# Kernel tuning notes

Measured on AMD Instinct MI355X. Metric: run time of the kernel, lower is better.

The kernel has to match this reference:

```python
import jax, jax.numpy as jnp
import numpy as np

N, IN_DIM, OUT_DIM, NUM_HOPS, SD = 8192, 256, 256, 4, 64
ETA, LAM_LAP, LAM_SP, EPS = 0.5, 0.3, 0.05, 0.5
LN_EPS = 1e-5


def setup_inputs() -> dict:
    key = jax.random.key(0)
    ks = jax.random.split(key, 6)
    K = NUM_HOPS + 1
    return {
        "H": jax.random.normal(ks[0], (N, IN_DIM), jnp.float32),
        "hops": jax.random.normal(ks[1], (K, N, IN_DIM), jnp.float32),
        "L": jax.random.normal(ks[2], (N, N), jnp.float32),
        "U": jax.random.normal(ks[3], (K, IN_DIM, SD), jnp.float32) * 0.1,
        "W_in": jax.random.normal(ks[4], (OUT_DIM, IN_DIM), jnp.float32) * 0.05,
        "ln_gamma": jnp.ones((OUT_DIM,), jnp.float32),
        "ln_beta": jnp.zeros((OUT_DIM,), jnp.float32),
        "log_tau": jnp.zeros((), jnp.float32),
    }


def _per_hop(U_k, H_k):
    n = H_k.shape[0]
    Q, _ = jnp.linalg.qr(U_k)                 # [in_dim, sd]
    Z = Q.T @ H_k.T                           # [sd, n]
    G = Z @ Z.T                               # [sd, sd] Gram, reused
    Sigma = G / (n + 1e-8)
    tr_S = jnp.trace(Sigma)
    tr_S2 = jnp.sum(Sigma * Sigma)            # trace(Sigma @ Sigma), Sigma symmetric
    rank_eff = tr_S ** 2 / (tr_S2 + 1e-8)
    coeff = SD / (n * EPS ** 2 + 1e-8)
    M = jnp.eye(SD, dtype=Z.dtype) + coeff * G
    Lc = jnp.linalg.cholesky(M)
    MiZ = jax.scipy.linalg.cho_solve((Lc, True), Z)  # [sd, n]
    grad_R = (Q @ MiZ).T                      # [n, in_dim]
    return rank_eff, grad_R


def reference(H, hops, L, U, W_in, ln_gamma, ln_beta, log_tau):
    tau = jnp.clip(jnp.exp(log_tau), 0.1, 10.0)
    rank_effs, grads_R = jax.vmap(_per_hop)(U, hops)      # [K], [K,n,in_dim]
    lap_terms = jnp.einsum('nm,kmd->knd', L, hops)        # [K,n,in_dim]
    w = jax.nn.softmax(rank_effs / tau)                   # [K]
    grad_sum = jnp.einsum('k,knd->nd', w, grads_R)
    lap_sum = jnp.einsum('k,knd->nd', w, lap_terms)
    H_half = H + ETA * grad_sum - ETA * LAM_LAP * lap_sum
    H_prox = jnp.sign(H_half) * jax.nn.relu(jnp.abs(H_half) - LAM_SP * ETA)
    H_out = H_prox @ W_in.T
    mu = jnp.mean(H_out, axis=-1, keepdims=True)
    var = jnp.var(H_out, axis=-1, keepdims=True)
    H_out = (H_out - mu) * jax.lax.rsqrt(var + LN_EPS) * ln_gamma + ln_beta
    return H_out, rank_effs, w
```

## Files before the change

kernel.cpp:

```cpp
#include <hip/hip_runtime.h>
#include <stdint.h>


typedef __attribute__((ext_vector_type(8))) short  s16x8;
typedef __attribute__((ext_vector_type(4))) float  f32x4;

#define NNODE 8192
#define DIN   256
#define KHOP  5
#define SDM   64

static const size_t OFF_Q    = 0;
static const size_t OFF_QT   = OFF_Q   + (size_t)5*256*64*4;
static const size_t OFF_ZT   = OFF_QT  + (size_t)5*64*256*2;
static const size_t OFF_GP   = OFF_ZT  + (size_t)5*8192*64*2;
static const size_t OFF_LM   = OFF_GP  + (size_t)5*16*4096*4;
static const size_t OFF_RD   = OFF_LM  + (size_t)5*4096*4;
static const size_t OFF_LU   = OFF_RD  + (size_t)5*64*4;
static const size_t OFF_RDU  = OFF_LU  + (size_t)5*4096*4;
static const size_t OFF_RE   = OFF_RDU + (size_t)5*64*4;
static const size_t OFF_W    = OFF_RE  + 64;
static const size_t OFF_T2   = OFF_W   + 64;
static const size_t OFF_HWT  = OFF_T2  + (size_t)5*256*64*2;
static const size_t OFF_WBF  = OFF_HWT + (size_t)256*8192*2;
static const size_t OFF_HP   = OFF_WBF + (size_t)256*256*2;
static const size_t OFF_PART = OFF_HP  + (size_t)8192*256*2;

__device__ __forceinline__ unsigned short f2bf(float f){
  unsigned u = __builtin_bit_cast(unsigned, f);
  u += 0x7FFFu + ((u >> 16) & 1u);
  return (unsigned short)(u >> 16);
}
__device__ __forceinline__ float bf2f(unsigned h){
  return __builtin_bit_cast(float, h << 16);
}
__device__ __forceinline__ void gl_lds16(const void* g, void* l){
  __builtin_amdgcn_global_load_lds(
      (const __attribute__((address_space(1))) void*)g,
      (__attribute__((address_space(3))) void*)l, 16, 0, 0);
}
__device__ __forceinline__ f32x4 mfma16(s16x8 a, s16x8 b, f32x4 c){
  return __builtin_amdgcn_mfma_f32_16x16x32_bf16(a, b, c, 0, 0, 0);
}
__device__ __forceinline__ int swz(int row7, int colbyte){
  return row7*128 + (colbyte ^ (row7 << 4));
}

__device__ __forceinline__ void wave_chol64(float* a, float& rdk, int lane){
  rdk = 0.0f;
  #pragma unroll
  for (int j = 0; j < 64; ++j){
    float dj  = __shfl(a[j], j);
    float d   = sqrtf(fmaxf(dj, 1e-20f));
    float rdj = 1.0f / d;
    float cj  = a[j] * rdj;
    a[j] = cj;
    if (lane == j) rdk = rdj;
    #pragma unroll
    for (int l = j+1; l < 64; ++l)
      a[l] -= cj * __shfl(cj, l);
  }
}

__global__ __launch_bounds__(256) void k_pre(const float* __restrict__ U,
                                             float* __restrict__ Lu,
                                             float* __restrict__ rdu){
  __shared__ float A[64*65];
  int tid = threadIdx.x;
  int k = blockIdx.x;
  const float* Uk = U + (size_t)k*16384;
  int ti = tid >> 4, tj = tid & 15;
  float s[16];
  #pragma unroll
  for (int i = 0; i < 16; ++i) s[i] = 0.0f;
  for (int n = 0; n < 256; ++n){
    f32x4 xa = *(const f32x4*)(Uk + n*64 + ti*4);
    f32x4 xb = *(const f32x4*)(Uk + n*64 + tj*4);
    #pragma unroll
    for (int p = 0; p < 4; ++p)
      #pragma unroll
      for (int q = 0; q < 4; ++q) s[p*4+q] += xa[p]*xb[q];
  }
  #pragma unroll
  for (int p = 0; p < 4; ++p)
    #pragma unroll
    for (int q = 0; q < 4; ++q) A[(ti*4+p)*65 + tj*4+q] = s[p*4+q];
  __syncthreads();
  if (tid < 64){
    int lane = tid;
    float a[64];
    #pragma unroll
    for (int l = 0; l < 64; ++l) a[l] = A[lane*65 + l];
    float rdk;
    wave_chol64(a, rdk, lane);
    #pragma unroll
    for (int l = 0; l < 64; ++l) Lu[(size_t)k*4096 + lane*64 + l] = a[l];
    rdu[k*64 + lane] = rdk;
  }
}

__global__ __launch_bounds__(256) void k_qsolve(const float* __restrict__ U,
                                                const float* __restrict__ Lu,
                                                const float* __restrict__ rdu,
                                                float* __restrict__ Qf,
                                                unsigned short* __restrict__ Qt){
  int k = blockIdx.y, tid = threadIdx.x, wave = tid >> 6, lane = tid & 63;
  __shared__ float Al[64*65];
  __shared__ float rds[64];
  for (int e = tid; e < 4096; e += 256) Al[(e>>6)*65 + (e&63)] = Lu[(size_t)k*4096 + e];
  if (tid < 64) rds[tid] = rdu[k*64 + tid];
  __syncthreads();
  int n = blockIdx.x*4 + wave;
  float x = U[((size_t)k*256 + n)*64 + lane];
  #pragma unroll
  for (int j = 0; j < 64; ++j){
    float zj = __shfl(x, j) * rds[j];
    x = (lane == j) ? zj : (lane > j ? x - Al[lane*65+j]*zj : x);
  }
  Qf[((size_t)k*256 + n)*64 + lane] = x;
  Qt[(size_t)k*16384 + lane*256 + n] = f2bf(x);
}

__global__ __launch_bounds__(256,2) void k_zgemm(const float* __restrict__ hops,
                                                 const unsigned short* __restrict__ Qt,
                                                 unsigned short* __restrict__ Zt){
  __shared__ __align__(16) unsigned short Al[128][72];
  __shared__ __align__(16) unsigned short Bl[64][64];
  int tid = threadIdx.x, lane = tid & 63, wave = tid >> 6;
  int q = lane >> 4, r = lane & 15;
  int k = blockIdx.y, m0 = blockIdx.x * 128;
  f32x4 acc[2][4];
  #pragma unroll
  for (int a = 0; a < 2; ++a)
    #pragma unroll
    for (int b = 0; b < 4; ++b) acc[a][b] = (f32x4){0,0,0,0};
  int rr = tid >> 1, half = tid & 1;
  for (int it = 0; it < 4; ++it){
    __syncthreads();
    #pragma unroll
    for (int i = 0; i < 2; ++i){
      int o = i*4096 + wave*1024 + lane*16;
      int srow = o >> 7, kc = (o & 127) >> 1;
      gl_lds16(Qt + (size_t)k*16384 + srow*256 + it*64 + kc,
               (char*)&Bl[0][0] + i*4096 + wave*1024);
    }
    const float* ga = hops + ((size_t)k*NNODE + m0 + rr)*256 + it*64 + half*32;
    f32x4 v[8];
    #pragma unroll
    for (int i = 0; i < 8; ++i) v[i] = *(const f32x4*)(ga + i*4);
    #pragma unroll
    for (int i = 0; i < 4; ++i){
      s16x8 t;
      #pragma unroll
      for (int j = 0; j < 8; ++j){ int e = i*8+j; t[j] = (short)f2bf(v[e>>2][e&3]); }
      *(s16x8*)&Al[rr][half*32 + i*8] = t;
    }
    __syncthreads();
    #pragma unroll
    for (int h = 0; h < 2; ++h){
      int ko = h*32 + q*8;
      s16x8 b[4];
      #pragma unroll
      for (int ni = 0; ni < 4; ++ni) b[ni] = *(const s16x8*)&Bl[ni*16 + r][ko];
      #pragma unroll
      for (int mi = 0; mi < 2; ++mi){
        s16x8 a = *(const s16x8*)&Al[wave*32 + mi*16 + r][ko];
        #pragma unroll
        for (int ni = 0; ni < 4; ++ni) acc[mi][ni] = mfma16(a, b[ni], acc[mi][ni]);
      }
    }
  }
  #pragma unroll
  for (int mi = 0; mi < 2; ++mi)
    #pragma unroll
    for (int ni = 0; ni < 4; ++ni)
      #pragma unroll
      for (int ii = 0; ii < 4; ++ii){
        int m = m0 + wave*32 + mi*16 + q*4 + ii;
        int sc = ni*16 + r;
        Zt[((size_t)k*NNODE + m)*64 + sc] = f2bf(acc[mi][ni][ii]);
      }
}

__global__ __launch_bounds__(256) void k_gpart(const unsigned short* __restrict__ Zt,
                                               float* __restrict__ Gp){
  int k = blockIdx.x, c = blockIdx.y, tid = threadIdx.x;
  __shared__ __align__(16) unsigned short Zl[128][64];
  int ti = tid >> 4, tj = tid & 15;
  float acc[16];
  #pragma unroll
  for (int i = 0; i < 16; ++i) acc[i] = 0.0f;
  for (int sub = 0; sub < 4; ++sub){
    const char* gb = (const char*)Zt + ((size_t)k*NNODE + c*512 + sub*128)*128;
    __syncthreads();
    #pragma unroll
    for (int i = 0; i < 4; ++i){
      int o = i*4096 + tid*16;
      *(uint4*)((char*)&Zl[0][0] + o) = *(const uint4*)(gb + o);
    }
    __syncthreads();
    for (int n = 0; n < 128; ++n){
      const unsigned short* row = &Zl[n][0];
      uint2 ua = *(const uint2*)(row + ti*4);
      uint2 ub = *(const uint2*)(row + tj*4);
      float xa[4] = { bf2f(ua.x & 0xffff), bf2f(ua.x >> 16), bf2f(ua.y & 0xffff), bf2f(ua.y >> 16) };
      float xb[4] = { bf2f(ub.x & 0xffff), bf2f(ub.x >> 16), bf2f(ub.y & 0xffff), bf2f(ub.y >> 16) };
      #pragma unroll
      for (int p = 0; p < 4; ++p)
        #pragma unroll
        for (int qn = 0; qn < 4; ++qn) acc[p*4+qn] += xa[p]*xb[qn];
    }
  }
  float* o = Gp + ((size_t)k*16 + c)*4096;
  #pragma unroll
  for (int p = 0; p < 4; ++p)
    #pragma unroll
    for (int qn = 0; qn < 4; ++qn) o[(ti*4+p)*64 + tj*4+qn] = acc[p*4+qn];
}

__global__ __launch_bounds__(256) void k_gred(const float* __restrict__ Gp,
                                              float* __restrict__ LmO,
                                              float* __restrict__ rdO,
                                              float* __restrict__ reO){
  int k = blockIdx.x, tid = threadIdx.x;
  __shared__ float A[64*65];
  __shared__ float red[256];
  int ti = tid >> 4, tj = tid & 15;
  float s[16];
  #pragma unroll
  for (int i = 0; i < 16; ++i) s[i] = 0.0f;
  for (int c = 0; c < 16; ++c){
    const float* g = Gp + ((size_t)k*16 + c)*4096 + (ti*4)*64 + tj*4;
    #pragma unroll
    for (int p = 0; p < 4; ++p)
      #pragma unroll
      for (int qn = 0; qn < 4; ++qn) s[p*4+qn] += g[p*64+qn];
  }
  const float sc    = 1.0f / (8192.0f + 1e-8f);
  const float coeff = 64.0f / (8192.0f*0.25f + 1e-8f);
  float trp = 0.0f, tr2p = 0.0f;
  #pragma unroll
  for (int p = 0; p < 4; ++p)
    #pragma unroll
    for (int qn = 0; qn < 4; ++qn){
      float gg = s[p*4+qn];
      float sg = gg * sc;
      tr2p += sg*sg;
      int row = ti*4+p, col = tj*4+qn;
      if (row == col) trp += sg;
      A[row*65 + col] = (row == col ? 1.0f : 0.0f) + coeff*gg;
    }
  red[tid] = trp; __syncthreads();
  for (int o = 128; o > 0; o >>= 1){ if (tid < o) red[tid] += red[tid+o]; __syncthreads(); }
  float tr = red[0]; __syncthreads();
  red[tid] = tr2p; __syncthreads();
  for (int o = 128; o > 0; o >>= 1){ if (tid < o) red[tid] += red[tid+o]; __syncthreads(); }
  float tr2 = red[0];
  if (tid == 0) reO[k] = tr*tr / (tr2 + 1e-8f);
  __syncthreads();
  if (tid < 64){
    int lane = tid;
    float a[64];
    #pragma unroll
    for (int l = 0; l < 64; ++l) a[l] = A[lane*65 + l];
    float rdk;
    wave_chol64(a, rdk, lane);
    #pragma unroll
    for (int l = 0; l < 64; ++l) LmO[(size_t)k*4096 + lane*64 + l] = a[l];
    rdO[k*64 + lane] = rdk;
  }
}

__global__ void k_soft(const float* __restrict__ re, const float* __restrict__ ltau,
                       float* __restrict__ wv, float* __restrict__ dtail){
  if (threadIdx.x == 0){
    float tau = expf(ltau[0]);
    tau = fminf(fmaxf(tau, 0.1f), 10.0f);
    float r[5], m = -1e30f;
    for (int i = 0; i < 5; ++i){ r[i] = re[i]; m = fmaxf(m, r[i]); }
    float e[5], sum = 0.0f;
    for (int i = 0; i < 5; ++i){ e[i] = expf((r[i]-m)/tau); sum += e[i]; }
    for (int i = 0; i < 5; ++i){
      float w = e[i]/sum;
      wv[i] = w; dtail[i] = r[i]; dtail[5+i] = w;
    }
  }
}

__global__ __launch_bounds__(256) void k_post(const float* __restrict__ hops,
                                              const float* __restrict__ wv,
                                              unsigned short* __restrict__ hwT,
                                              const float* __restrict__ Qf,
                                              const float* __restrict__ LmI,
                                              const float* __restrict__ rdI,
                                              unsigned short* __restrict__ T2w,
                                              const float* __restrict__ Win,
                                              unsigned short* __restrict__ Wbf){
  __shared__ float T[64*65];
  __shared__ float rds[64];
  int bid = blockIdx.x, tid = threadIdx.x;
  if (bid < 512){
    int n0 = (bid & 127)*64, d0 = (bid >> 7)*64;
    float wl[5];
    #pragma unroll
    for (int k = 0; k < 5; ++k) wl[k] = -0.15f * wv[k];
    for (int e = tid; e < 1024; e += 256){
      int row = e >> 4, c4 = (e & 15)*4;
      f32x4 acc = (f32x4){0,0,0,0};
      #pragma unroll
      for (int k = 0; k < 5; ++k){
        f32x4 v = *(const f32x4*)(hops + ((size_t)k*NNODE + n0 + row)*256 + d0 + c4);
        acc += v * wl[k];
      }
      T[row*65 + c4+0] = acc[0]; T[row*65 + c4+1] = acc[1];
      T[row*65 + c4+2] = acc[2]; T[row*65 + c4+3] = acc[3];
    }
    __syncthreads();
    for (int e = tid; e < 1024; e += 256){
      int dr = e >> 4, c4 = (e & 15)*4;
      unsigned short h0 = f2bf(T[(c4+0)*65 + dr]);
      unsigned short h1 = f2bf(T[(c4+1)*65 + dr]);
      unsigned short h2 = f2bf(T[(c4+2)*65 + dr]);
      unsigned short h3 = f2bf(T[(c4+3)*65 + dr]);
      uint2 u; u.x = (unsigned)h0 | ((unsigned)h1 << 16); u.y = (unsigned)h2 | ((unsigned)h3 << 16);
      *(uint2*)(hwT + (size_t)(d0+dr)*NNODE + n0 + c4) = u;
    }
  } else if (bid < 832){
    int i = bid - 512;
    int k = i >> 6, xb = i & 63;
    int wave = tid >> 6, lane = tid & 63;
    for (int e = tid; e < 4096; e += 256) T[(e>>6)*65 + (e&63)] = LmI[(size_t)k*4096 + e];
    if (tid < 64) rds[tid] = rdI[k*64 + tid];
    __syncthreads();
    int n = xb*4 + wave;
    float x = Qf[((size_t)k*256 + n)*64 + lane];
    #pragma unroll
    for (int j = 0; j < 64; ++j){
      float zj = __shfl(x, j) * rds[j];
      x = (lane == j) ? zj : (lane > j ? x - T[lane*65+j]*zj : x);
    }
    #pragma unroll
    for (int j = 63; j >= 0; --j){
      float yj = __shfl(x, j) * rds[j];
      x = (lane == j) ? yj : (lane < j ? x - T[j*65+lane]*yj : x);
    }
    float scale = 0.5f * wv[k];
    T2w[((size_t)k*256 + n)*64 + lane] = f2bf(scale * x);
  } else {
    int i = bid - 832;
    int e = (i*256 + tid)*4;
    f32x4 v = *(const f32x4*)(Win + e);
    uint2 u;
    u.x = (unsigned)f2bf(v[0]) | ((unsigned)f2bf(v[1]) << 16);
    u.y = (unsigned)f2bf(v[2]) | ((unsigned)f2bf(v[3]) << 16);
    *(uint2*)(Wbf + e) = u;
  }
}

__global__ __launch_bounds__(256,2) void k_gg(const float* __restrict__ Lf,
                                              const unsigned short* __restrict__ Bt,
                                              unsigned short* __restrict__ part,
                                              const unsigned short* __restrict__ Zt,
                                              const unsigned short* __restrict__ T2w){
  __shared__ __align__(16) unsigned short SM[24960];
  int bid = blockIdx.x, tid = threadIdx.x;
  int lane = tid & 63, wave = tid >> 6;
  int q = lane >> 4, r = lane & 15;
  if (bid < 512){
    char* Al = (char*)SM;
    char* Bl = (char*)SM + 16*1040;
    int m0 = (bid & 63) * 128;
    int by = bid >> 6;
    size_t kbase = (size_t)by * 1024;
    int sr = lane >> 3;
    int sc8b = ((lane & 7) ^ sr) * 8;
    int sc8a = (lane & 7) * 8;
    int adst = swz(sr, (lane & 7) * 16);
    f32x4 acc[8][4];
    #pragma unroll
    for (int a = 0; a < 8; ++a)
      #pragma unroll
      for (int b = 0; b < 4; ++b) acc[a][b] = (f32x4){0,0,0,0};
    {
      f32x4 av[4][2];
      #pragma unroll
      for (int i = 0; i < 4; ++i){
        int c = i*4 + wave;
        const float* p = Lf + (size_t)(m0 + c*8 + sr)*NNODE + kbase + sc8a;
        av[i][0] = *(const f32x4*)p;
        av[i][1] = *(const f32x4*)(p + 4);
      }
      #pragma unroll
      for (int i = 0; i < 8; ++i){
        int cb = i*4 + wave;
        gl_lds16(Bt + (size_t)(cb*8 + sr)*NNODE + kbase + sc8b,
                 Bl + cb*1040 + lane*16);
      }
      #pragma unroll
      for (int i = 0; i < 4; ++i){
        int c = i*4 + wave;
        s16x8 t;
        #pragma unroll
        for (int e = 0; e < 8; ++e) t[e] = (short)f2bf(av[i][e>>2][e&3]);
        *(s16x8*)(Al + c*1040 + adst) = t;
      }
      __syncthreads();
    }
    for (int t = 0; t < 16; ++t){
      size_t kn = kbase + (size_t)(t+1)*64;
      f32x4 av[4][2];
      if (t < 15){
        #pragma unroll
        for (int i = 0; i < 4; ++i){
          int c = i*4 + wave;
          const float* p = Lf + (size_t)(m0 + c*8 + sr)*NNODE + kn + sc8a;
          av[i][0] = *(const f32x4*)p;
          av[i][1] = *(const f32x4*)(p + 4);
        }
      }
      #pragma unroll
      for (int h = 0; h < 2; ++h){
        int kb = h*64 + q*16;
        s16x8 b[4];
        #pragma unroll
        for (int ni = 0; ni < 4; ++ni){
          int d = wave*64 + ni*16 + r;
          b[ni] = *(const s16x8*)(Bl + (d>>3)*1040 + swz(d&7, kb));
        }
        #pragma unroll
        for (int mi = 0; mi < 8; ++mi){
          int m = mi*16 + r;
          s16x8 a = *(const s16x8*)(Al + (m>>3)*1040 + swz(m&7, kb));
          #pragma unroll
          for (int ni = 0; ni < 4; ++ni) acc[mi][ni] = mfma16(a, b[ni], acc[mi][ni]);
        }
      }
      __syncthreads();
      if (t < 15){
        #pragma unroll
        for (int i = 0; i < 8; ++i){
          int cb = i*4 + wave;
          gl_lds16(Bt + (size_t)(cb*8 + sr)*NNODE + kn + sc8b,
                   Bl + cb*1040 + lane*16);
        }
        #pragma unroll
        for (int i = 0; i < 4; ++i){
          int c = i*4 + wave;
          s16x8 tt;
          #pragma unroll
          for (int e = 0; e < 8; ++e) tt[e] = (short)f2bf(av[i][e>>2][e&3]);
          *(s16x8*)(Al + c*1040 + adst) = tt;
        }
      }
      __syncthreads();
    }
    unsigned short* o = part + (size_t)by * 2097152;
    #pragma unroll
    for (int mi = 0; mi < 8; ++mi)
      #pragma unroll
      for (int ni = 0; ni < 4; ++ni)
        #pragma unroll
        for (int ii = 0; ii < 4; ++ii){
          int m = m0 + mi*16 + q*4 + ii;
          int n = wave*64 + ni*16 + r;
          o[(size_t)m*256 + n] = f2bf(acc[mi][ni][ii]);
        }
  } else {
    char* Al = (char*)SM;
    char* Bl = (char*)SM + 4096;
    int m0 = (bid - 512) * 32;
    int gr8 = lane >> 3;
    int gcS = ((lane & 7) ^ gr8) * 16;
    f32x4 acc[2][4];
    #pragma unroll
    for (int a = 0; a < 2; ++a)
      #pragma unroll
      for (int b = 0; b < 4; ++b) acc[a][b] = (f32x4){0,0,0,0};
    for (int kk = 0; kk < 5; ++kk){
      __syncthreads();
      {
        int grow = wave*8 + gr8;
        gl_lds16((const char*)Zt + ((size_t)kk*NNODE + m0 + grow)*128 + gcS,
                 Al + wave*1024);
      }
      #pragma unroll
      for (int i = 0; i < 8; ++i){
        int cb = i*4 + wave;
        int grow = cb*8 + gr8;
        gl_lds16((const char*)T2w + (size_t)kk*65536 + (size_t)grow*128 + gcS,
                 Bl + cb*1024 + wave*0 + lane*16 - lane*16 + lane*16);
      }
      __syncthreads();
      #pragma unroll
      for (int h = 0; h < 2; ++h){
        int kb = h*64 + q*16;
        s16x8 b[4];
        #pragma unroll
        for (int ni = 0; ni < 4; ++ni){
          int row = wave*64 + ni*16 + r;
          b[ni] = *(const s16x8*)(Bl + (row>>3)*1024 + swz(row&7, kb));
        }
        #pragma unroll
        for (int mi = 0; mi < 2; ++mi){
          int row = mi*16 + r;
          s16x8 a = *(const s16x8*)(Al + (row>>3)*1024 + swz(row&7, kb));
          #pragma unroll
          for (int ni = 0; ni < 4; ++ni) acc[mi][ni] = mfma16(a, b[ni], acc[mi][ni]);
        }
      }
    }
    unsigned short* o8 = part + (size_t)8 * 2097152;
    #pragma unroll
    for (int mi = 0; mi < 2; ++mi)
      #pragma unroll
      for (int ni = 0; ni < 4; ++ni)
        #pragma unroll
        for (int ii = 0; ii < 4; ++ii){
          int m = m0 + mi*16 + q*4 + ii;
          int n = wave*64 + ni*16 + r;
          o8[(size_t)m*256 + n] = f2bf(acc[mi][ni][ii]);
        }
  }
}

__global__ __launch_bounds__(256,2) void k_finln(const float* __restrict__ H,
                                                 const unsigned short* __restrict__ part,
                                                 const unsigned short* __restrict__ Wbf,
                                                 const float* __restrict__ gamma,
                                                 const float* __restrict__ beta,
                                                 float* __restrict__ out){
  __shared__ __align__(16) unsigned short Hl[64][264];
  __shared__ __align__(16) unsigned short Bl[256][64];
  __shared__ float SmR[64][4];
  __shared__ float SqR[64][4];
  int tid = threadIdx.x, lane = tid & 63, wave = tid >> 6;
  int q = lane >> 4, r = lane & 15;
  int m0 = blockIdx.x * 64;
  #define PROX(a) ({ float _t = fabsf(a) - 0.025f; _t > 0.0f ? copysignf(_t,(a)) : 0.0f; })
  for (int g = tid; g < 4096; g += 256){
    int row = g >> 6, c4 = (g & 63) * 4;
    size_t e = (size_t)(m0 + row)*256 + c4;
    f32x4 h = *(const f32x4*)(H + e);
    float s0 = h[0], s1 = h[1], s2 = h[2], s3 = h[3];
    #pragma unroll
    for (int sl = 0; sl < 9; ++sl){
      uint2 u = *(const uint2*)(part + (size_t)sl*2097152 + e);
      s0 += bf2f(u.x & 0xffff); s1 += bf2f(u.x >> 16);
      s2 += bf2f(u.y & 0xffff); s3 += bf2f(u.y >> 16);
    }
    uint2 o;
    o.x = (unsigned)f2bf(PROX(s0)) | ((unsigned)f2bf(PROX(s1)) << 16);
    o.y = (unsigned)f2bf(PROX(s2)) | ((unsigned)f2bf(PROX(s3)) << 16);
    *(uint2*)&Hl[row][c4] = o;
  }
  f32x4 acc[4][4];
  #pragma unroll
  for (int a = 0; a < 4; ++a)
    #pragma unroll
    for (int b = 0; b < 4; ++b) acc[a][b] = (f32x4){0,0,0,0};
  for (int it = 0; it < 4; ++it){
    __syncthreads();
    #pragma unroll
    for (int i = 0; i < 8; ++i){
      int o = i*4096 + wave*1024 + lane*16;
      int n = o >> 7, kc = o & 127;
      gl_lds16((const char*)Wbf + (size_t)n*512 + it*128 + kc,
               (char*)&Bl[0][0] + i*4096 + wave*1024);
    }
    __syncthreads();
    #pragma unroll
    for (int h = 0; h < 2; ++h){
      int ko = it*64 + h*32 + q*8;
      s16x8 b[4];
      #pragma unroll
      for (int ni = 0; ni < 4; ++ni) b[ni] = *(const s16x8*)&Bl[wave*64 + ni*16 + r][h*32 + q*8];
      #pragma unroll
      for (int mi = 0; mi < 4; ++mi){
        s16x8 a = *(const s16x8*)&Hl[mi*16 + r][ko];
        #pragma unroll
        for (int ni = 0; ni < 4; ++ni) acc[mi][ni] = mfma16(a, b[ni], acc[mi][ni]);
      }
    }
  }
  #pragma unroll
  for (int mi = 0; mi < 4; ++mi)
    #pragma unroll
    for (int ii = 0; ii < 4; ++ii){
      float sm = 0.0f, sq = 0.0f;
      #pragma unroll
      for (int ni = 0; ni < 4; ++ni){
        float v = acc[mi][ni][ii];
        sm += v; sq += v*v;
      }
      #pragma unroll
      for (int o = 1; o < 16; o <<= 1){ sm += __shfl_xor(sm, o, 64); sq += __shfl_xor(sq, o, 64); }
      if (r == 0){
        int rl = mi*16 + q*4 + ii;
        SmR[rl][wave] = sm; SqR[rl][wave] = sq;
      }
    }
  __syncthreads();
  float g[4], b[4];
  #pragma unroll
  for (int ni = 0; ni < 4; ++ni){
    g[ni] = gamma[wave*64 + ni*16 + r];
    b[ni] = beta [wave*64 + ni*16 + r];
  }
  #pragma unroll
  for (int mi = 0; mi < 4; ++mi)
    #pragma unroll
    for (int ii = 0; ii < 4; ++ii){
      int rl = mi*16 + q*4 + ii;
      float sm = SmR[rl][0] + SmR[rl][1] + SmR[rl][2] + SmR[rl][3];
      float sq = SqR[rl][0] + SqR[rl][1] + SqR[rl][2] + SqR[rl][3];
      float mean = sm * (1.0f/256.0f);
      float var  = sq * (1.0f/256.0f) - mean*mean;
      float rs   = rsqrtf(var + 1e-5f);
      #pragma unroll
      for (int ni = 0; ni < 4; ++ni){
        out[(size_t)(m0+rl)*256 + wave*64 + ni*16 + r] =
            (acc[mi][ni][ii] - mean)*rs*g[ni] + b[ni];
      }
    }
}

extern "C" void kernel_launch(void* const* d_in, const int* in_sizes, int n_in,
                              void* d_out, int out_size, void* d_ws, size_t ws_size,
                              hipStream_t stream){
  const float* H    = (const float*)d_in[0];
  const float* hops = (const float*)d_in[1];
  const float* Lmat = (const float*)d_in[2];
  const float* U    = (const float*)d_in[3];
  const float* Win  = (const float*)d_in[4];
  const float* gam  = (const float*)d_in[5];
  const float* bet  = (const float*)d_in[6];
  const float* ltau = (const float*)d_in[7];
  float* out = (float*)d_out;

  char* ws = (char*)d_ws;
  float*          Qf   = (float*)(ws + OFF_Q);
  unsigned short* Qt   = (unsigned short*)(ws + OFF_QT);
  unsigned short* Zt   = (unsigned short*)(ws + OFF_ZT);
  float*          Gp   = (float*)(ws + OFF_GP);
  float*          Lm   = (float*)(ws + OFF_LM);
  float*          rdw  = (float*)(ws + OFF_RD);
  float*          Lu   = (float*)(ws + OFF_LU);
  float*          rdu  = (float*)(ws + OFF_RDU);
  float*          re   = (float*)(ws + OFF_RE);
  float*          wv   = (float*)(ws + OFF_W);
  unsigned short* T2w  = (unsigned short*)(ws + OFF_T2);
  unsigned short* hwT  = (unsigned short*)(ws + OFF_HWT);
  unsigned short* Wbf  = (unsigned short*)(ws + OFF_WBF);
  unsigned short* part = (unsigned short*)(ws + OFF_PART);

  hipLaunchKernelGGL(k_pre,    dim3(5),      dim3(256), 0, stream, U, Lu, rdu);
  hipLaunchKernelGGL(k_qsolve, dim3(64,5),   dim3(256), 0, stream, U, Lu, rdu, Qf, Qt);
  hipLaunchKernelGGL(k_zgemm,  dim3(64,5),   dim3(256), 0, stream, hops, Qt, Zt);
  hipLaunchKernelGGL(k_gpart,  dim3(5,16),   dim3(256), 0, stream, Zt, Gp);
  hipLaunchKernelGGL(k_gred,   dim3(5),      dim3(256), 0, stream, Gp, Lm, rdw, re);
  hipLaunchKernelGGL(k_soft,   dim3(1),      dim3(64),  0, stream, re, ltau, wv, out + 2097152);
  hipLaunchKernelGGL(k_post,   dim3(896),    dim3(256), 0, stream, hops, wv, hwT, Qf, Lm, rdw, T2w, Win, Wbf);
  hipLaunchKernelGGL(k_gg,     dim3(768),    dim3(256), 0, stream, Lmat, hwT, part, Zt, T2w);
  hipLaunchKernelGGL(k_finln,  dim3(128),    dim3(256), 0, stream, H, part, Wbf, gam, bet, out);
}
```

Before: 647.7 us.

## Split fused GEMM kernel and use eight-wave 64x64 tiles for the L GEMM

Splits the combined GEMM kernel in two. The small per-hop gradient GEMM becomes its own launch, and the large L·hops GEMM becomes a 512-thread kernel. There, each of eight waves computes a 64x64 sub-tile of the 128x256 block instead of four waves each doing 128x64. This halves per-thread accumulator registers and spreads staging loads across more waves to improve latency hiding. It also corrects the per-hop stride into T2w from 65536 to 32768 bytes, which makes the gradient GEMM read the right hop slice. The cost is an extra kernel launch, and the two GEMMs now run back to back instead of sharing one grid.

```diff
diff --git a/kernel.cpp b/kernel.cpp
--- a/kernel.cpp
+++ b/kernel.cpp
@@ -357,170 +357,172 @@
   }
 }
 
-__global__ __launch_bounds__(256,2) void k_gg(const float* __restrict__ Lf,
-                                              const unsigned short* __restrict__ Bt,
-                                              unsigned short* __restrict__ part,
-                                              const unsigned short* __restrict__ Zt,
-                                              const unsigned short* __restrict__ T2w){
+__global__ __launch_bounds__(256,2) void k_grad(const unsigned short* __restrict__ Zt,
+                                                const unsigned short* __restrict__ T2w,
+                                                unsigned short* __restrict__ out8){
+  __shared__ __align__(16) unsigned short SM[18432];
+  char* Al = (char*)SM;
+  char* Bl = (char*)SM + 4096;
+  int tid = threadIdx.x, lane = tid & 63, wave = tid >> 6;
+  int q = lane >> 4, r = lane & 15;
+  int m0 = blockIdx.x * 32;
+  int gr8 = lane >> 3;
+  int gcS = ((lane & 7) ^ gr8) * 16;
+  f32x4 acc[2][4];
+  #pragma unroll
+  for (int a = 0; a < 2; ++a)
+    #pragma unroll
+    for (int b = 0; b < 4; ++b) acc[a][b] = (f32x4){0,0,0,0};
+  for (int kk = 0; kk < 5; ++kk){
+    __syncthreads();
+    {
+      int grow = wave*8 + gr8;
+      gl_lds16((const char*)Zt + ((size_t)kk*NNODE + m0 + grow)*128 + gcS,
+               Al + wave*1024);
+    }
+    #pragma unroll
+    for (int i = 0; i < 8; ++i){
+      int cb = i*4 + wave;
+      int grow = cb*8 + gr8;
+      gl_lds16((const char*)T2w + (size_t)kk*32768 + (size_t)grow*128 + gcS,
+               Bl + cb*1024);
+    }
+    __syncthreads();
+    #pragma unroll
+    for (int h = 0; h < 2; ++h){
+      int kb = h*64 + q*16;
+      s16x8 b[4];
+      #pragma unroll
+      for (int ni = 0; ni < 4; ++ni){
+        int row = wave*64 + ni*16 + r;
+        b[ni] = *(const s16x8*)(Bl + (row>>3)*1024 + swz(row&7, kb));
+      }
+      #pragma unroll
+      for (int mi = 0; mi < 2; ++mi){
+        int row = mi*16 + r;
+        s16x8 a = *(const s16x8*)(Al + (row>>3)*1024 + swz(row&7, kb));
+        #pragma unroll
+        for (int ni = 0; ni < 4; ++ni) acc[mi][ni] = mfma16(a, b[ni], acc[mi][ni]);
+      }
+    }
+  }
+  #pragma unroll
+  for (int mi = 0; mi < 2; ++mi)
+    #pragma unroll
+    for (int ni = 0; ni < 4; ++ni)
+      #pragma unroll
+      for (int ii = 0; ii < 4; ++ii){
+        int m = m0 + mi*16 + q*4 + ii;
+        int n = wave*64 + ni*16 + r;
+        out8[(size_t)m*256 + n] = f2bf(acc[mi][ni][ii]);
+      }
+}
+
+__global__ __launch_bounds__(512,1) void k_big(const float* __restrict__ Lf,
+                                               const unsigned short* __restrict__ Bt,
+                                               unsigned short* __restrict__ part){
   __shared__ __align__(16) unsigned short SM[24960];
-  int bid = blockIdx.x, tid = threadIdx.x;
-  int lane = tid & 63, wave = tid >> 6;
+  char* Al = (char*)SM;
+  char* Bl = (char*)SM + 16*1040;
+  int tid = threadIdx.x, lane = tid & 63, wave = tid >> 6;
   int q = lane >> 4, r = lane & 15;
-  if (bid < 512){
-    char* Al = (char*)SM;
-    char* Bl = (char*)SM + 16*1040;
-    int m0 = (bid & 63) * 128;
-    int by = bid >> 6;
-    size_t kbase = (size_t)by * 1024;
-    int sr = lane >> 3;
-    int sc8b = ((lane & 7) ^ sr) * 8;
-    int sc8a = (lane & 7) * 8;
-    int adst = swz(sr, (lane & 7) * 16);
-    f32x4 acc[8][4];
-    #pragma unroll
-    for (int a = 0; a < 8; ++a)
-      #pragma unroll
-      for (int b = 0; b < 4; ++b) acc[a][b] = (f32x4){0,0,0,0};
-    {
-      f32x4 av[4][2];
-      #pragma unroll
-      for (int i = 0; i < 4; ++i){
-        int c = i*4 + wave;
-        const float* p = Lf + (size_t)(m0 + c*8 + sr)*NNODE + kbase + sc8a;
+  int wr = wave >> 2, wc = wave & 3;
+  int m0 = (blockIdx.x & 63) * 128;
+  int by = blockIdx.x >> 6;
+  size_t kbase = (size_t)by * 1024;
+  int sr = lane >> 3;
+  int sc8b = ((lane & 7) ^ sr) * 8;
+  int sc8a = (lane & 7) * 8;
+  int adst = swz(sr, (lane & 7) * 16);
+  f32x4 acc[4][4];
+  #pragma unroll
+  for (int a = 0; a < 4; ++a)
+    #pragma unroll
+    for (int b = 0; b < 4; ++b) acc[a][b] = (f32x4){0,0,0,0};
+  {
+    f32x4 av[2][2];
+    #pragma unroll
+    for (int i = 0; i < 2; ++i){
+      int c = wave*2 + i;
+      const float* p = Lf + (size_t)(m0 + c*8 + sr)*NNODE + kbase + sc8a;
+      av[i][0] = *(const f32x4*)p;
+      av[i][1] = *(const f32x4*)(p + 4);
+    }
+    #pragma unroll
+    for (int i = 0; i < 4; ++i){
+      int cb = wave*4 + i;
+      gl_lds16(Bt + (size_t)(cb*8 + sr)*NNODE + kbase + sc8b,
+               Bl + cb*1040);
+    }
+    #pragma unroll
+    for (int i = 0; i < 2; ++i){
+      int c = wave*2 + i;
+      s16x8 t;
+      #pragma unroll
+      for (int e = 0; e < 8; ++e) t[e] = (short)f2bf(av[i][e>>2][e&3]);
+      *(s16x8*)(Al + c*1040 + adst) = t;
+    }
+    __syncthreads();
+  }
+  for (int t = 0; t < 16; ++t){
+    size_t kn = kbase + (size_t)(t+1)*64;
+    f32x4 av[2][2];
+    if (t < 15){
+      #pragma unroll
+      for (int i = 0; i < 2; ++i){
+        int c = wave*2 + i;
+        const float* p = Lf + (size_t)(m0 + c*8 + sr)*NNODE + kn + sc8a;
         av[i][0] = *(const f32x4*)p;
         av[i][1] = *(const f32x4*)(p + 4);
       }
-      #pragma unroll
-      for (int i = 0; i < 8; ++i){
-        int cb = i*4 + wave;
-        gl_lds16(Bt + (size_t)(cb*8 + sr)*NNODE + kbase + sc8b,
-                 Bl + cb*1040 + lane*16);
-      }
+    }
+    #pragma unroll
+    for (int h = 0; h < 2; ++h){
+      int kb = h*64 + q*16;
+      s16x8 b[4];
+      #pragma unroll
+      for (int ni = 0; ni < 4; ++ni){
+        int d = wc*64 + ni*16 + r;
+        b[ni] = *(const s16x8*)(Bl + (d>>3)*1040 + swz(d&7, kb));
+      }
+      #pragma unroll
+      for (int mi = 0; mi < 4; ++mi){
+        int m = wr*64 + mi*16 + r;
+        s16x8 a = *(const s16x8*)(Al + (m>>3)*1040 + swz(m&7, kb));
+        #pragma unroll
+        for (int ni = 0; ni < 4; ++ni) acc[mi][ni] = mfma16(a, b[ni], acc[mi][ni]);
+      }
+    }
+    __syncthreads();
+    if (t < 15){
       #pragma unroll
       for (int i = 0; i < 4; ++i){
-        int c = i*4 + wave;
-        s16x8 t;
+        int cb = wave*4 + i;
+        gl_lds16(Bt + (size_t)(cb*8 + sr)*NNODE + kn + sc8b,
+                 Bl + cb*1040);
+      }
+      #pragma unroll
+      for (int i = 0; i < 2; ++i){
+        int c = wave*2 + i;
+        s16x8 tt;
         #pragma unroll
-        for (int e = 0; e < 8; ++e) t[e] = (short)f2bf(av[i][e>>2][e&3]);
-        *(s16x8*)(Al + c*1040 + adst) = t;
-      }
-      __syncthreads();
-    }
-    for (int t = 0; t < 16; ++t){
-      size_t kn = kbase + (size_t)(t+1)*64;
-      f32x4 av[4][2];
-      if (t < 15){
-        #pragma unroll
-        for (int i = 0; i < 4; ++i){
-          int c = i*4 + wave;
-          const float* p = Lf + (size_t)(m0 + c*8 + sr)*NNODE + kn + sc8a;
-          av[i][0] = *(const f32x4*)p;
-          av[i][1] = *(const f32x4*)(p + 4);
-        }
-      }
-      #pragma unroll
-      for (int h = 0; h < 2; ++h){
-        int kb = h*64 + q*16;
-        s16x8 b[4];
-        #pragma unroll
-        for (int ni = 0; ni < 4; ++ni){
-          int d = wave*64 + ni*16 + r;
-          b[ni] = *(const s16x8*)(Bl + (d>>3)*1040 + swz(d&7, kb));
-        }
-        #pragma unroll
-        for (int mi = 0; mi < 8; ++mi){
-          int m = mi*16 + r;
-          s16x8 a = *(const s16x8*)(Al + (m>>3)*1040 + swz(m&7, kb));
-          #pragma unroll
-          for (int ni = 0; ni < 4; ++ni) acc[mi][ni] = mfma16(a, b[ni], acc[mi][ni]);
-        }
-      }
-      __syncthreads();
-      if (t < 15){
-        #pragma unroll
-        for (int i = 0; i < 8; ++i){
-          int cb = i*4 + wave;
-          gl_lds16(Bt + (size_t)(cb*8 + sr)*NNODE + kn + sc8b,
-                   Bl + cb*1040 + lane*16);
-        }
-        #pragma unroll
-        for (int i = 0; i < 4; ++i){
-          int c = i*4 + wave;
-          s16x8 tt;
-          #pragma unroll
-          for (int e = 0; e < 8; ++e) tt[e] = (short)f2bf(av[i][e>>2][e&3]);
-          *(s16x8*)(Al + c*1040 + adst) = tt;
-        }
-      }
-      __syncthreads();
-    }
-    unsigned short* o = part + (size_t)by * 2097152;
-    #pragma unroll
-    for (int mi = 0; mi < 8; ++mi)
-      #pragma unroll
-      for (int ni = 0; ni < 4; ++ni)
-        #pragma unroll
-        for (int ii = 0; ii < 4; ++ii){
-          int m = m0 + mi*16 + q*4 + ii;
-          int n = wave*64 + ni*16 + r;
-          o[(size_t)m*256 + n] = f2bf(acc[mi][ni][ii]);
-        }
-  } else {
-    char* Al = (char*)SM;
-    char* Bl = (char*)SM + 4096;
-    int m0 = (bid - 512) * 32;
-    int gr8 = lane >> 3;
-    int gcS = ((lane & 7) ^ gr8) * 16;
-    f32x4 acc[2][4];
-    #pragma unroll
-    for (int a = 0; a < 2; ++a)
-      #pragma unroll
-      for (int b = 0; b < 4; ++b) acc[a][b] = (f32x4){0,0,0,0};
-    for (int kk = 0; kk < 5; ++kk){
-      __syncthreads();
-      {
-        int grow = wave*8 + gr8;
-        gl_lds16((const char*)Zt + ((size_t)kk*NNODE + m0 + grow)*128 + gcS,
-                 Al + wave*1024);
-      }
-      #pragma unroll
-      for (int i = 0; i < 8; ++i){
-        int cb = i*4 + wave;
-        int grow = cb*8 + gr8;
-        gl_lds16((const char*)T2w + (size_t)kk*65536 + (size_t)grow*128 + gcS,
-                 Bl + cb*1024 + wave*0 + lane*16 - lane*16 + lane*16);
-      }
-      __syncthreads();
-      #pragma unroll
-      for (int h = 0; h < 2; ++h){
-        int kb = h*64 + q*16;
-        s16x8 b[4];
-        #pragma unroll
-        for (int ni = 0; ni < 4; ++ni){
-          int row = wave*64 + ni*16 + r;
-          b[ni] = *(const s16x8*)(Bl + (row>>3)*1024 + swz(row&7, kb));
-        }
-        #pragma unroll
-        for (int mi = 0; mi < 2; ++mi){
-          int row = mi*16 + r;
-          s16x8 a = *(const s16x8*)(Al + (row>>3)*1024 + swz(row&7, kb));
-          #pragma unroll
-          for (int ni = 0; ni < 4; ++ni) acc[mi][ni] = mfma16(a, b[ni], acc[mi][ni]);
-        }
-      }
-    }
-    unsigned short* o8 = part + (size_t)8 * 2097152;
-    #pragma unroll
-    for (int mi = 0; mi < 2; ++mi)
-      #pragma unroll
-      for (int ni = 0; ni < 4; ++ni)
-        #pragma unroll
-        for (int ii = 0; ii < 4; ++ii){
-          int m = m0 + mi*16 + q*4 + ii;
-          int n = wave*64 + ni*16 + r;
-          o8[(size_t)m*256 + n] = f2bf(acc[mi][ni][ii]);
-        }
-  }
+        for (int e = 0; e < 8; ++e) tt[e] = (short)f2bf(av[i][e>>2][e&3]);
+        *(s16x8*)(Al + c*1040 + adst) = tt;
+      }
+    }
+    __syncthreads();
+  }
+  unsigned short* o = part + (size_t)by * 2097152;
+  #pragma unroll
+  for (int mi = 0; mi < 4; ++mi)
+    #pragma unroll
+    for (int ni = 0; ni < 4; ++ni)
+      #pragma unroll
+      for (int ii = 0; ii < 4; ++ii){
+        int m = m0 + wr*64 + mi*16 + q*4 + ii;
+        int n = wc*64 + ni*16 + r;
+        o[(size_t)m*256 + n] = f2bf(acc[mi][ni][ii]);
+      }
 }
 
 __global__ __launch_bounds__(256,2) void k_finln(const float* __restrict__ H,
@@ -660,6 +662,7 @@
   hipLaunchKernelGGL(k_gred,   dim3(5),      dim3(256), 0, stream, Gp, Lm, rdw, re);
   hipLaunchKernelGGL(k_soft,   dim3(1),      dim3(64),  0, stream, re, ltau, wv, out + 2097152);
   hipLaunchKernelGGL(k_post,   dim3(896),    dim3(256), 0, stream, hops, wv, hwT, Qf, Lm, rdw, T2w, Win, Wbf);
-  hipLaunchKernelGGL(k_gg,     dim3(768),    dim3(256), 0, stream, Lmat, hwT, part, Zt, T2w);
+  hipLaunchKernelGGL(k_grad,   dim3(256),    dim3(256), 0, stream, Zt, T2w, part + (size_t)8*2097152);
+  hipLaunchKernelGGL(k_big,    dim3(512),    dim3(512), 0, stream, Lmat, hwT, part);
   hipLaunchKernelGGL(k_finln,  dim3(128),    dim3(256), 0, stream, H, part, Wbf, gam, bet, out);
 }
```

After: 649.2 us. About the same (+0.2%).
